# Kernel tuning notes

Measured on AMD Instinct MI355X. Metric: run time of the kernel, lower is better.

## Reference

```python
import jax, jax.numpy as jnp
import numpy as np

N = 50000
E = 800000
G = 256          # number of graphs in the batch
F_IN = 128
H1, D1 = 12, 32  # conv1: heads, out-per-head (concat -> 384)
H2, D2 = 1, 64   # conv2: single head
NEG_SLOPE = 0.2


def setup_inputs() -> dict:
    key = jax.random.key(0)
    ks = jax.random.split(key, 12)
    x = jax.random.normal(ks[0], (N, F_IN), dtype=jnp.float32)
    edge_index = jax.random.randint(ks[1], (2, E), 0, N, dtype=jnp.int64)
    batch = jnp.sort(jax.random.randint(ks[2], (N,), 0, G, dtype=jnp.int64))
    # conv1 params (Glorot-ish scaling)
    W1 = jax.random.normal(ks[3], (F_IN, H1 * D1), dtype=jnp.float32) * (1.0 / np.sqrt(F_IN))
    att_src1 = jax.random.normal(ks[4], (H1, D1), dtype=jnp.float32) * (1.0 / np.sqrt(D1))
    att_dst1 = jax.random.normal(ks[5], (H1, D1), dtype=jnp.float32) * (1.0 / np.sqrt(D1))
    bias1 = jnp.zeros((H1 * D1,), dtype=jnp.float32)
    # conv2 params
    W2 = jax.random.normal(ks[6], (H1 * D1, H2 * D2), dtype=jnp.float32) * (1.0 / np.sqrt(H1 * D1))
    att_src2 = jax.random.normal(ks[7], (H2, D2), dtype=jnp.float32) * (1.0 / np.sqrt(D2))
    att_dst2 = jax.random.normal(ks[8], (H2, D2), dtype=jnp.float32) * (1.0 / np.sqrt(D2))
    bias2 = jnp.zeros((H2 * D2,), dtype=jnp.float32)
    return {"x": x, "edge_index": edge_index, "batch": batch,
            "W1": W1, "att_src1": att_src1, "att_dst1": att_dst1, "bias1": bias1,
            "W2": W2, "att_src2": att_src2, "att_dst2": att_dst2, "bias2": bias2}


def gat_conv(x, src, dst, W, att_src, att_dst, bias, heads, d_out):
    # x: [N, F] -> h: [N, heads, d_out]
    h = (x @ W).reshape(N, heads, d_out)
    # per-node attention halves: [N, heads]
    a_src = jnp.einsum('nhd,hd->nh', h, att_src)
    a_dst = jnp.einsum('nhd,hd->nh', h, att_dst)
    # per-edge logits (edges include self-loops): [Etot, heads]
    e = jax.nn.leaky_relu(a_src[src] + a_dst[dst], NEG_SLOPE)
    # segment softmax over incoming edges of each destination node
    m = jax.ops.segment_max(e, dst, num_segments=N)          # [N, heads]
    e = jnp.exp(e - m[dst])
    s = jax.ops.segment_sum(e, dst, num_segments=N)          # [N, heads]
    alpha = e / s[dst]
    # weighted aggregation: [N, heads, d_out]
    out = jax.ops.segment_sum(alpha[:, :, None] * h[src], dst, num_segments=N)
    return out.reshape(N, heads * d_out) + bias


def reference(x, edge_index, batch, W1, att_src1, att_dst1, bias1,
              W2, att_src2, att_dst2, bias2):
    # add self-loops (PyG GATConv default add_self_loops=True)
    loops = jnp.arange(N, dtype=edge_index.dtype)
    src = jnp.concatenate([edge_index[0], loops])
    dst = jnp.concatenate([edge_index[1], loops])

    h = jax.nn.relu(gat_conv(x, src, dst, W1, att_src1, att_dst1, bias1, H1, D1))
    h = gat_conv(h, src, dst, W2, att_src2, att_dst2, bias2, H2, D2)

    # global mean pool over graphs
    sums = jax.ops.segment_sum(h, batch, num_segments=G)                 # [G, 64]
    cnts = jax.ops.segment_sum(jnp.ones((N,), h.dtype), batch, num_segments=G)
    return sums / jnp.maximum(cnts, 1.0)[:, None]
```

## Files before the change

kernel.cpp:

```cpp
#include <hip/hip_runtime.h>

#define N_NODES 50000
#define N_EDGES 800000
#define ETOT (N_EDGES + N_NODES)
#define G_GRAPHS 256
#define F_IN 128
#define H1 12
#define D1 32
#define C1 (H1*D1)
#define C2 64
#define NEG 0.2f
#define SCAN_B 1024
#define NBLK_SCAN ((N_NODES + SCAN_B - 1)/SCAN_B)

using bf16x8  = __attribute__((ext_vector_type(8))) short;
using ushort8 = __attribute__((ext_vector_type(8))) unsigned short;
using f32x4   = __attribute__((ext_vector_type(4))) float;

__device__ __forceinline__ float lrelu(float x){ return x > 0.f ? x : NEG*x; }
__device__ __forceinline__ unsigned short f2bf(float f){
  unsigned u = __float_as_uint(f);
  u += 0x7fffu + ((u >> 16) & 1u);
  return (unsigned short)(u >> 16);
}
__device__ __forceinline__ float bf2f(unsigned short h){
  return __uint_as_float(((unsigned)h) << 16);
}
__device__ __forceinline__ float wexp(float l){ return __expf(fminf(l, 30.f)); }

#define B_CAST ((N_NODES*F_IN/4 + 255)/256)
#define B_W1   ((F_IN*C1 + 255)/256)
#define B_W2   ((C1*C2 + 255)/256)
#define B_WAB  ((32*F_IN + 255)/256)
__global__ void prep_kernel(const float* __restrict__ x, const float* __restrict__ W1,
    const float* __restrict__ W2, const float* __restrict__ att_src,
    const float* __restrict__ att_dst, unsigned short* __restrict__ xb,
    unsigned short* __restrict__ w1t, unsigned short* __restrict__ w2t,
    unsigned short* __restrict__ wAb){
  int b = blockIdx.x, tid = threadIdx.x;
  if (b < B_CAST){
    int base = (b*256 + tid)*4;
    if (base >= N_NODES*F_IN) return;
    float4 v = *(const float4*)(x + base);
    ushort4 o; o.x=f2bf(v.x); o.y=f2bf(v.y); o.z=f2bf(v.z); o.w=f2bf(v.w);
    *(ushort4*)(xb + base) = o;
  } else if (b < B_CAST + B_W1){
    int i = (b - B_CAST)*256 + tid;
    if (i >= F_IN*C1) return;
    int n = i / F_IN, k = i % F_IN;
    w1t[i] = f2bf(W1[(size_t)k*C1 + n]);
  } else if (b < B_CAST + B_W1 + B_W2){
    int i = (b - B_CAST - B_W1)*256 + tid;
    if (i >= C1*C2) return;
    int n = i / C1, k = i % C1;
    w2t[i] = f2bf(W2[(size_t)k*C2 + n]);
  } else {
    int i = (b - B_CAST - B_W1 - B_W2)*256 + tid;
    if (i >= 32*F_IN) return;
    int c = i >> 7, k = i & 127;
    float v = 0.f;
    if (c < 12){
      #pragma unroll
      for (int dd=0; dd<D1; ++dd) v += W1[(size_t)k*C1 + c*D1 + dd] * att_src[c*D1 + dd];
    } else if (c < 24){
      int h = c - 12;
      #pragma unroll
      for (int dd=0; dd<D1; ++dd) v += W1[(size_t)k*C1 + h*D1 + dd] * att_dst[h*D1 + dd];
    }
    wAb[i] = f2bf(v);
  }
}

template<int BM,int BN,int WM,int WN,bool F32OUT>
__global__ __launch_bounds__(256) void gemm_mfma(const unsigned short* __restrict__ A,
    const unsigned short* __restrict__ Bt, void* __restrict__ Cv,
    int M, int N, int K){
  constexpr int BK = 32;
  __shared__ unsigned short As2[4][BM][8];
  __shared__ unsigned short Bs2[4][BN][8];
  const int tid  = threadIdx.x;
  const int wid  = tid >> 6, lane = tid & 63;
  constexpr int NWX = BN / WN;
  const int wrow = (wid / NWX) * WM, wcol = (wid % NWX) * WN;
  constexpr int MR = WM/16, NR = WN/16;
  const int row0 = blockIdx.x * BM, col0 = blockIdx.y * BN;
  const int r = lane & 15, koct = lane >> 4;
  f32x4 acc[MR][NR];
  #pragma unroll
  for (int m=0;m<MR;m++)
    #pragma unroll
    for (int n=0;n<NR;n++) acc[m][n] = f32x4{0.f,0.f,0.f,0.f};

  for (int k0 = 0; k0 < K; k0 += BK){
    for (int s = tid; s < BM*8; s += 256){
      int rr = s >> 3, cc = (s & 7) * 4;
      int gr = row0 + rr;
      ushort4 v = (gr < M) ? *(const ushort4*)(A + (size_t)gr*K + k0 + cc)
                           : ushort4{0,0,0,0};
      *(ushort4*)(&As2[cc>>3][rr][cc&7]) = v;
    }
    for (int s = tid; s < BN*8; s += 256){
      int rr = s >> 3, cc = (s & 7) * 4;
      ushort4 v = *(const ushort4*)(Bt + (size_t)(col0+rr)*K + k0 + cc);
      *(ushort4*)(&Bs2[cc>>3][rr][cc&7]) = v;
    }
    __syncthreads();
    bf16x8 af[MR], bq[NR];
    #pragma unroll
    for (int m=0;m<MR;m++) af[m] = *(const bf16x8*)(&As2[koct][wrow + m*16 + r][0]);
    #pragma unroll
    for (int n=0;n<NR;n++) bq[n] = *(const bf16x8*)(&Bs2[koct][wcol + n*16 + r][0]);
    #pragma unroll
    for (int m=0;m<MR;m++)
      #pragma unroll
      for (int n=0;n<NR;n++)
        acc[m][n] = __builtin_amdgcn_mfma_f32_16x16x32_bf16(af[m], bq[n], acc[m][n], 0,0,0);
    __syncthreads();
  }
  #pragma unroll
  for (int m=0;m<MR;m++){
    #pragma unroll
    for (int rr=0; rr<4; rr++){
      int grow = row0 + wrow + m*16 + koct*4 + rr;
      if (grow < M){
        #pragma unroll
        for (int n=0;n<NR;n++){
          if constexpr (F32OUT)
            ((float*)Cv)[(size_t)grow*N + col0 + wcol + n*16 + r] = acc[m][n][rr];
          else
            ((unsigned short*)Cv)[(size_t)grow*N + col0 + wcol + n*16 + r] = f2bf(acc[m][n][rr]);
        }
      }
    }
  }
}

#define EGRID ((ETOT + 255)/256)
#define NGRID ((N_NODES + 255)/256)
__global__ void count_cnt_kernel(const int* __restrict__ ei, const int* __restrict__ batch,
                                 int* __restrict__ counts, int* __restrict__ cnt){
  if ((int)blockIdx.x < EGRID){
    int e = blockIdx.x*256 + threadIdx.x;
    if (e >= ETOT) return;
    int d = (e < N_EDGES) ? ei[N_EDGES + e] : (e - N_EDGES);
    atomicAdd(&counts[d], 1);
  } else {
    int n = (blockIdx.x - EGRID)*256 + threadIdx.x;
    if (n < N_NODES) atomicAdd(&cnt[batch[n]], 1);
  }
}
__global__ __launch_bounds__(SCAN_B) void scan_pass1(const int* __restrict__ counts,
    int* __restrict__ excl, int* __restrict__ bsum){
  __shared__ int sdata[SCAN_B];
  int i = blockIdx.x*SCAN_B + threadIdx.x;
  int v = (i < N_NODES) ? counts[i] : 0;
  sdata[threadIdx.x] = v;
  __syncthreads();
  for (int off=1; off<SCAN_B; off<<=1){
    int t = (threadIdx.x >= off) ? sdata[threadIdx.x-off] : 0;
    __syncthreads();
    sdata[threadIdx.x] += t;
    __syncthreads();
  }
  if (i < N_NODES) excl[i] = sdata[threadIdx.x] - v;
  if (threadIdx.x == SCAN_B-1) bsum[blockIdx.x] = sdata[SCAN_B-1];
}
__global__ void scan_pass3(int* __restrict__ rowptr, const int* __restrict__ bsum,
                           int* __restrict__ cursor){
  __shared__ int carry_s;
  int sblk = blockIdx.x >> 2;
  if (threadIdx.x == 0){
    int c = 0;
    for (int b=0; b<sblk; ++b) c += bsum[b];
    carry_s = c;
  }
  __syncthreads();
  int i = blockIdx.x*256 + (int)threadIdx.x;
  if (i < N_NODES){
    int r = rowptr[i] + carry_s;
    rowptr[i] = r; cursor[i] = r;
  }
  if (i == N_NODES) rowptr[N_NODES] = ETOT;
}
__global__ void scatter_kernel(const int* __restrict__ ei, int* __restrict__ cursor,
                               int* __restrict__ csr_src){
  int e = blockIdx.x*blockDim.x + threadIdx.x;
  if (e >= ETOT) return;
  int s, d;
  if (e < N_EDGES){ s = ei[e]; d = ei[N_EDGES + e]; } else { s = d = e - N_EDGES; }
  int slot = atomicAdd(&cursor[d], 1);
  csr_src[slot] = s;
}

__global__ __launch_bounds__(256) void agg1g_kernel(const int* __restrict__ rowptr,
    const int* __restrict__ csr, const unsigned short* __restrict__ xb,
    const float* __restrict__ asd, const unsigned short* __restrict__ w1t,
    const unsigned short* __restrict__ w2t, const float* __restrict__ bias1,
    const float* __restrict__ att_src2, const float* __restrict__ att_dst2,
    unsigned short* __restrict__ h2, float* __restrict__ asrc2, float* __restrict__ adst2){
  constexpr int ROWE = 6*F_IN + 8;
  constexpr int WROW = 16*12 + 4;
  constexpr int ROWR = 192 + 8;
  __shared__ unsigned short agg[16*ROWE];
  __shared__ float wlds[16][WROW];

  unsigned short* reluLDS = (unsigned short*)&wlds[0][0];
  float* red = (float*)&agg[0];

  const int tid  = threadIdx.x;
  const int slot = tid >> 4;
  const int t16  = tid & 15;
  const int base = ((tid & 63) >> 4) * 16;
  const int d    = blockIdx.x*16 + slot;
  const int r0 = rowptr[d], r1 = rowptr[d+1];

  float4 ad0 = *(const float4*)(asd + (size_t)d*32 + 12);
  float4 ad1 = *(const float4*)(asd + (size_t)d*32 + 16);
  float4 ad2 = *(const float4*)(asd + (size_t)d*32 + 20);
  float ad[12] = {ad0.x,ad0.y,ad0.z,ad0.w, ad1.x,ad1.y,ad1.z,ad1.w, ad2.x,ad2.y,ad2.z,ad2.w};

  float acc[12][8];
  #pragma unroll
  for (int h=0;h<12;h++)
    #pragma unroll
    for (int i=0;i<8;i++) acc[h][i] = 0.f;
  float ss[12];
  #pragma unroll
  for (int h=0;h<12;h++) ss[h] = 0.f;

  for (int c0 = r0; c0 < r1; c0 += 16){
    int nc = min(16, r1 - c0);
    int s_st = 0;
    if (t16 < nc){
      int j = c0 + t16;
      s_st = csr[j];
      float4 s0 = *(const float4*)(asd + (size_t)s_st*32);
      float4 s1 = *(const float4*)(asd + (size_t)s_st*32 + 4);
      float4 s2 = *(const float4*)(asd + (size_t)s_st*32 + 8);
      float as[12] = {s0.x,s0.y,s0.z,s0.w, s1.x,s1.y,s1.z,s1.w, s2.x,s2.y,s2.z,s2.w};
      float w[12];
      #pragma unroll
      for (int h=0;h<12;h++){ w[h] = wexp(lrelu(as[h] + ad[h])); ss[h] += w[h]; }
      *(float4*)(&wlds[slot][t16*12 + 0]) = float4{w[0],w[1],w[2],w[3]};
      *(float4*)(&wlds[slot][t16*12 + 4]) = float4{w[4],w[5],w[6],w[7]};
      *(float4*)(&wlds[slot][t16*12 + 8]) = float4{w[8],w[9],w[10],w[11]};
    }
    __builtin_amdgcn_wave_barrier();
    int sA = __shfl(s_st, base + 0);
    ushort8 xA = *(const ushort8*)(xb + (size_t)sA*F_IN + t16*8);
    ushort8 xB = {0,0,0,0,0,0,0,0};
    if (nc > 1){
      int sB = __shfl(s_st, base + 1);
      xB = *(const ushort8*)(xb + (size_t)sB*F_IN + t16*8);
    }
    for (int e = 0; e < nc; ++e){
      ushort8 cx = xA;
      xA = xB;
      if (e + 2 < nc){
        int sN = __shfl(s_st, base + e + 2);
        xB = *(const ushort8*)(xb + (size_t)sN*F_IN + t16*8);
      }
      float4 w0 = *(const float4*)(&wlds[slot][e*12 + 0]);
      float4 w1 = *(const float4*)(&wlds[slot][e*12 + 4]);
      float4 w2 = *(const float4*)(&wlds[slot][e*12 + 8]);
      float xf[8];
      #pragma unroll
      for (int i=0;i<8;i++) xf[i] = bf2f((unsigned short)cx[i]);
      float w[12] = {w0.x,w0.y,w0.z,w0.w, w1.x,w1.y,w1.z,w1.w, w2.x,w2.y,w2.z,w2.w};
      #pragma unroll
      for (int h=0;h<12;h++)
        #pragma unroll
        for (int i=0;i<8;i++) acc[h][i] += w[h]*xf[i];
    }
    __builtin_amdgcn_wave_barrier();
  }

  #pragma unroll
  for (int h=0;h<12;h++){
    #pragma unroll
    for (int off=8; off; off>>=1) ss[h] += __shfl_xor(ss[h], off);
  }
  float inv[12];
  #pragma unroll
  for (int h=0;h<12;h++) inv[h] = 1.f / ss[h];

  const int wv = tid >> 6, wl = tid & 63;
  const int er = wl & 15, eq = wl >> 4;
  f32x4 h2acc = {0.f,0.f,0.f,0.f};
  #pragma unroll
  for (int hf = 0; hf < 2; ++hf){
    __syncthreads();
    #pragma unroll
    for (int h = 0; h < 6; ++h){
      int hh = hf*6 + h;
      ushort8 v;
      #pragma unroll
      for (int i=0;i<8;i++) v[i] = f2bf(acc[hh][i]*inv[hh]);
      *(ushort8*)(&agg[slot*ROWE + h*F_IN + t16*8]) = v;
    }
    __syncthreads();
    for (int tt = wv; tt < 12; tt += 4){
      int h = tt >> 1, nb = tt & 1;
      int hh = hf*6 + h;
      f32x4 c = {0.f,0.f,0.f,0.f};
      #pragma unroll
      for (int kk=0; kk<4; ++kk){
        bf16x8 af = *(const bf16x8*)(&agg[er*ROWE + h*F_IN + kk*32 + eq*8]);
        bf16x8 bq = *(const bf16x8*)(w1t + (size_t)(hh*32 + nb*16 + er)*F_IN + kk*32 + eq*8);
        c = __builtin_amdgcn_mfma_f32_16x16x32_bf16(af, bq, c, 0,0,0);
      }
      int lcol = tt*16 + er;
      float bv = bias1[hf*192 + lcol];
      #pragma unroll
      for (int rr=0; rr<4; ++rr){
        int row = eq*4 + rr;
        reluLDS[row*ROWR + lcol] = f2bf(fmaxf(c[rr] + bv, 0.f));
      }
    }
    __syncthreads();
    #pragma unroll
    for (int kk=0; kk<6; ++kk){
      bf16x8 af = *(const bf16x8*)(&reluLDS[er*ROWR + kk*32 + eq*8]);
      bf16x8 bq = *(const bf16x8*)(w2t + (size_t)(wv*16 + er)*C1 + hf*192 + kk*32 + eq*8);
      h2acc = __builtin_amdgcn_mfma_f32_16x16x32_bf16(af, bq, h2acc, 0,0,0);
    }
  }
  __syncthreads();

  float attS = att_src2[wv*16 + er];
  float attD = att_dst2[wv*16 + er];
  float psum[4], pdum[4];
  #pragma unroll
  for (int rr=0; rr<4; ++rr){
    int row = eq*4 + rr;
    int gn = blockIdx.x*16 + row;
    h2[(size_t)gn*C2 + wv*16 + er] = f2bf(h2acc[rr]);
    psum[rr] = h2acc[rr]*attS;
    pdum[rr] = h2acc[rr]*attD;
  }
  #pragma unroll
  for (int rr=0; rr<4; ++rr){
    #pragma unroll
    for (int off=8; off; off>>=1){
      psum[rr] += __shfl_xor(psum[rr], off);
      pdum[rr] += __shfl_xor(pdum[rr], off);
    }
  }
  if (er == 0){
    #pragma unroll
    for (int rr=0; rr<4; ++rr){
      int row = eq*4 + rr;
      red[(wv*16 + row)*2 + 0] = psum[rr];
      red[(wv*16 + row)*2 + 1] = pdum[rr];
    }
  }
  __syncthreads();
  if (tid < 32){
    int row = tid >> 1, which = tid & 1;
    float v = red[row*2+which] + red[(16+row)*2+which] + red[(32+row)*2+which] + red[(48+row)*2+which];
    int gn = blockIdx.x*16 + row;
    if (which == 0) asrc2[gn] = v; else adst2[gn] = v;
  }
}

__global__ __launch_bounds__(256) void agg2s_kernel(const int* __restrict__ rowptr,
    const int* __restrict__ csr, const unsigned short* __restrict__ h2,
    const float* __restrict__ asrc, const float* __restrict__ adst,
    const float* __restrict__ bias, const int* __restrict__ batch,
    float* __restrict__ pool){
  const int tid  = threadIdx.x;
  const int slot = tid >> 4;
  const int t16  = tid & 15;
  const int base = ((tid & 63) >> 4) * 16;
  const int d    = blockIdx.x*16 + slot;
  const int r0 = rowptr[d], r1 = rowptr[d+1];
  const float ad = adst[d];

  float ssp = 0.f;
  float a0=0.f, a1=0.f, a2=0.f, a3=0.f;

  for (int c0 = r0; c0 < r1; c0 += 16){
    int nc = min(16, r1 - c0);
    int s_st = 0; float w_st = 0.f;
    if (t16 < nc){
      s_st = csr[c0 + t16];
      w_st = wexp(lrelu(asrc[s_st] + ad));
      ssp += w_st;
    }
    int sA = __shfl(s_st, base + 0);
    ushort4 xA = *(const ushort4*)(h2 + (size_t)sA*C2 + t16*4);
    ushort4 xB = {0,0,0,0};
    if (nc > 1){
      int sB = __shfl(s_st, base + 1);
      xB = *(const ushort4*)(h2 + (size_t)sB*C2 + t16*4);
    }
    for (int e = 0; e < nc; ++e){
      ushort4 cx = xA;
      xA = xB;
      if (e + 2 < nc){
        int sN = __shfl(s_st, base + e + 2);
        xB = *(const ushort4*)(h2 + (size_t)sN*C2 + t16*4);
      }
      float w = __shfl(w_st, base + e);
      a0 += w*bf2f(cx.x);
      a1 += w*bf2f(cx.y);
      a2 += w*bf2f(cx.z);
      a3 += w*bf2f(cx.w);
    }
  }
  #pragma unroll
  for (int off=8; off; off>>=1) ssp += __shfl_xor(ssp, off);
  float inv = 1.f / ssp;
  int g = batch[d];
  int fb = t16*4;
  atomicAdd(&pool[g*C2 + fb+0], a0*inv + bias[fb+0]);
  atomicAdd(&pool[g*C2 + fb+1], a1*inv + bias[fb+1]);
  atomicAdd(&pool[g*C2 + fb+2], a2*inv + bias[fb+2]);
  atomicAdd(&pool[g*C2 + fb+3], a3*inv + bias[fb+3]);
}

__global__ void finalize_kernel(const float* __restrict__ sums, const int* __restrict__ cnt,
                                float* __restrict__ out){
  int i = blockIdx.x*blockDim.x + threadIdx.x;
  if (i >= G_GRAPHS*C2) return;
  int g = i >> 6;
  out[i] = sums[i] / fmaxf((float)cnt[g], 1.f);
}

extern "C" void kernel_launch(void* const* d_in, const int* in_sizes, int n_in,
                              void* d_out, int out_size, void* d_ws, size_t ws_size,
                              hipStream_t stream) {
  const float* x        = (const float*)d_in[0];
  const int*   ei       = (const int*)  d_in[1];
  const int*   batch    = (const int*)  d_in[2];
  const float* W1       = (const float*)d_in[3];
  const float* att_src1 = (const float*)d_in[4];
  const float* att_dst1 = (const float*)d_in[5];
  const float* bias1    = (const float*)d_in[6];
  const float* W2       = (const float*)d_in[7];
  const float* att_src2 = (const float*)d_in[8];
  const float* att_dst2 = (const float*)d_in[9];
  const float* bias2    = (const float*)d_in[10];
  float* out = (float*)d_out;

  char* ws = (char*)d_ws;
  size_t o = 0;
  auto alloc = [&](size_t bytes)->size_t{ size_t r=o; o=(o+bytes+255)&~(size_t)255; return r; };

  size_t xb_o     = alloc((size_t)N_NODES*F_IN*2);
  size_t w1t_o    = alloc((size_t)C1*F_IN*2);
  size_t w2t_o    = alloc((size_t)C2*C1*2);
  size_t wab_o    = alloc((size_t)32*F_IN*2);
  size_t asd_o    = alloc((size_t)N_NODES*32*4);
  size_t h2_o     = alloc((size_t)N_NODES*C2*2);
  size_t asrc2_o  = alloc((size_t)N_NODES*4);
  size_t adst2_o  = alloc((size_t)N_NODES*4);
  size_t zero_beg = o;
  size_t counts_o = alloc((size_t)N_NODES*4);
  size_t pool_o   = alloc((size_t)G_GRAPHS*C2*4);
  size_t cnt_o    = alloc((size_t)G_GRAPHS*4);
  size_t zero_end = o;
  size_t rowptr_o = alloc((size_t)(N_NODES+1)*4);
  size_t bsum_o   = alloc((size_t)NBLK_SCAN*4);
  size_t cursor_o = alloc((size_t)N_NODES*4);
  size_t csr_o    = alloc((size_t)ETOT*4);

  unsigned short* xb    = (unsigned short*)(ws + xb_o);
  unsigned short* w1t   = (unsigned short*)(ws + w1t_o);
  unsigned short* w2t   = (unsigned short*)(ws + w2t_o);
  unsigned short* wab   = (unsigned short*)(ws + wab_o);
  float* asd    = (float*)(ws + asd_o);
  unsigned short* h2b   = (unsigned short*)(ws + h2_o);
  float* asrc2  = (float*)(ws + asrc2_o);
  float* adst2  = (float*)(ws + adst2_o);
  int*   counts = (int*)  (ws + counts_o);
  float* poolf  = (float*)(ws + pool_o);
  int*   cnt    = (int*)  (ws + cnt_o);
  int*   rowptr = (int*)  (ws + rowptr_o);
  int*   bsum   = (int*)  (ws + bsum_o);
  int*   cursor = (int*)  (ws + cursor_o);
  int*   csrsrc = (int*)  (ws + csr_o);

  hipMemsetAsync(ws + zero_beg, 0, zero_end - zero_beg, stream);

  const int TPB = 256;

  prep_kernel<<<B_CAST + B_W1 + B_W2 + B_WAB, TPB, 0, stream>>>(
      x, W1, W2, att_src1, att_dst1, xb, w1t, w2t, wab);

  count_cnt_kernel<<<EGRID + NGRID, TPB, 0, stream>>>(ei, batch, counts, cnt);
  scan_pass1<<<NBLK_SCAN, SCAN_B, 0, stream>>>(counts, rowptr, bsum);
  scan_pass3<<<(N_NODES + 1 + 255)/256, TPB, 0, stream>>>(rowptr, bsum, cursor);
  scatter_kernel<<<EGRID, TPB, 0, stream>>>(ei, cursor, csrsrc);

  gemm_mfma<64,32,32,16,true><<<dim3((N_NODES+63)/64, 1), 256, 0, stream>>>(xb, wab, asd, N_NODES, 32, F_IN);
  agg1g_kernel<<<N_NODES/16, 256, 0, stream>>>(rowptr, csrsrc, xb, asd, w1t, w2t,
                                               bias1, att_src2, att_dst2, h2b, asrc2, adst2);
  agg2s_kernel<<<(N_NODES+15)/16, TPB, 0, stream>>>(rowptr, csrsrc, h2b, asrc2, adst2, bias2, batch, poolf);

  finalize_kernel<<<(G_GRAPHS*C2 + TPB-1)/TPB, TPB, 0, stream>>>(poolf, cnt, out);
}
```

Baseline: 424.4 us.

## Use MFMA for conv1 edge aggregation with one wave per destination node

The layer-1 aggregation kernel now assigns one 64-lane wave per destination node (1024-thread blocks, 16 nodes each) instead of 16 lanes per node. Each wave processes 32 edges per chunk. Gathered source features are transposed into swizzled LDS and reduced against bf16 attention weights with 16x16x32 bf16 MFMAs, replacing the scalar FMA accumulation over 12 heads by 8 features. The goal is to move the dominant per-edge weighted-sum work onto matrix cores. In exchange, attention weights are rounded to bf16, LDS use per block grows a lot, and zero-padding waste appears for low-degree nodes.

```diff
diff --git a/kernel.cpp b/kernel.cpp
--- a/kernel.cpp
+++ b/kernel.cpp
@@ -192,172 +192,188 @@
   csr_src[slot] = s;
 }
 
-__global__ __launch_bounds__(256) void agg1g_kernel(const int* __restrict__ rowptr,
+__global__ __launch_bounds__(1024) void agg1m_kernel(const int* __restrict__ rowptr,
     const int* __restrict__ csr, const unsigned short* __restrict__ xb,
     const float* __restrict__ asd, const unsigned short* __restrict__ w1t,
     const unsigned short* __restrict__ w2t, const float* __restrict__ bias1,
     const float* __restrict__ att_src2, const float* __restrict__ att_dst2,
     unsigned short* __restrict__ h2, float* __restrict__ asrc2, float* __restrict__ adst2){
-  constexpr int ROWE = 6*F_IN + 8;
-  constexpr int WROW = 16*12 + 4;
-  constexpr int ROWR = 192 + 8;
-  __shared__ unsigned short agg[16*ROWE];
-  __shared__ float wlds[16][WROW];
-
-  unsigned short* reluLDS = (unsigned short*)&wlds[0][0];
-  float* red = (float*)&agg[0];
+  __shared__ unsigned short XtU[16*128*32];
+  __shared__ unsigned short wldsU[16*16*32];
+  unsigned short* aggU  = XtU;
+  unsigned short* reluU = wldsU;
+  float* redF = (float*)&wldsU[7168];
 
   const int tid  = threadIdx.x;
-  const int slot = tid >> 4;
-  const int t16  = tid & 15;
-  const int base = ((tid & 63) >> 4) * 16;
-  const int d    = blockIdx.x*16 + slot;
+  const int wv   = tid >> 6;
+  const int lane = tid & 63;
+  const int e32  = lane & 31, half = lane >> 5;
+  const int r    = lane & 15, koct = lane >> 4;
+  const int d    = blockIdx.x*16 + wv;
   const int r0 = rowptr[d], r1 = rowptr[d+1];
+  const int wvX = wv * (128*32);
+  const int wvW = wv * (16*32);
+
+  if (lane < 32){
+    #pragma unroll
+    for (int h=12; h<16; ++h) wldsU[wvW + h*32 + lane] = 0;
+  }
 
   float4 ad0 = *(const float4*)(asd + (size_t)d*32 + 12);
   float4 ad1 = *(const float4*)(asd + (size_t)d*32 + 16);
   float4 ad2 = *(const float4*)(asd + (size_t)d*32 + 20);
   float ad[12] = {ad0.x,ad0.y,ad0.z,ad0.w, ad1.x,ad1.y,ad1.z,ad1.w, ad2.x,ad2.y,ad2.z,ad2.w};
 
-  float acc[12][8];
-  #pragma unroll
-  for (int h=0;h<12;h++)
-    #pragma unroll
-    for (int i=0;i<8;i++) acc[h][i] = 0.f;
+  f32x4 c[8];
+  #pragma unroll
+  for (int t=0;t<8;t++) c[t] = f32x4{0.f,0.f,0.f,0.f};
   float ss[12];
   #pragma unroll
   for (int h=0;h<12;h++) ss[h] = 0.f;
 
-  for (int c0 = r0; c0 < r1; c0 += 16){
-    int nc = min(16, r1 - c0);
+  for (int c0 = r0; c0 < r1; c0 += 32){
+    int nc = min(32, r1 - c0);
     int s_st = 0;
-    if (t16 < nc){
-      int j = c0 + t16;
-      s_st = csr[j];
-      float4 s0 = *(const float4*)(asd + (size_t)s_st*32);
-      float4 s1 = *(const float4*)(asd + (size_t)s_st*32 + 4);
-      float4 s2 = *(const float4*)(asd + (size_t)s_st*32 + 8);
-      float as[12] = {s0.x,s0.y,s0.z,s0.w, s1.x,s1.y,s1.z,s1.w, s2.x,s2.y,s2.z,s2.w};
-      float w[12];
-      #pragma unroll
-      for (int h=0;h<12;h++){ w[h] = wexp(lrelu(as[h] + ad[h])); ss[h] += w[h]; }
-      *(float4*)(&wlds[slot][t16*12 + 0]) = float4{w[0],w[1],w[2],w[3]};
-      *(float4*)(&wlds[slot][t16*12 + 4]) = float4{w[4],w[5],w[6],w[7]};
-      *(float4*)(&wlds[slot][t16*12 + 8]) = float4{w[8],w[9],w[10],w[11]};
+    if (lane < 32){
+      if (lane < nc){
+        s_st = csr[c0 + lane];
+        float4 s0 = *(const float4*)(asd + (size_t)s_st*32);
+        float4 s1 = *(const float4*)(asd + (size_t)s_st*32 + 4);
+        float4 s2 = *(const float4*)(asd + (size_t)s_st*32 + 8);
+        float as[12] = {s0.x,s0.y,s0.z,s0.w, s1.x,s1.y,s1.z,s1.w, s2.x,s2.y,s2.z,s2.w};
+        #pragma unroll
+        for (int h=0;h<12;h++){
+          unsigned short wb = f2bf(wexp(lrelu(as[h] + ad[h])));
+          wldsU[wvW + h*32 + lane] = wb;
+          ss[h] += bf2f(wb);
+        }
+      } else {
+        #pragma unroll
+        for (int h=0;h<12;h++) wldsU[wvW + h*32 + lane] = 0;
+      }
     }
     __builtin_amdgcn_wave_barrier();
-    int sA = __shfl(s_st, base + 0);
-    ushort8 xA = *(const ushort8*)(xb + (size_t)sA*F_IN + t16*8);
-    ushort8 xB = {0,0,0,0,0,0,0,0};
-    if (nc > 1){
-      int sB = __shfl(s_st, base + 1);
-      xB = *(const ushort8*)(xb + (size_t)sB*F_IN + t16*8);
-    }
-    for (int e = 0; e < nc; ++e){
-      ushort8 cx = xA;
-      xA = xB;
-      if (e + 2 < nc){
-        int sN = __shfl(s_st, base + e + 2);
-        xB = *(const ushort8*)(xb + (size_t)sN*F_IN + t16*8);
-      }
-      float4 w0 = *(const float4*)(&wlds[slot][e*12 + 0]);
-      float4 w1 = *(const float4*)(&wlds[slot][e*12 + 4]);
-      float4 w2 = *(const float4*)(&wlds[slot][e*12 + 8]);
-      float xf[8];
-      #pragma unroll
-      for (int i=0;i<8;i++) xf[i] = bf2f((unsigned short)cx[i]);
-      float w[12] = {w0.x,w0.y,w0.z,w0.w, w1.x,w1.y,w1.z,w1.w, w2.x,w2.y,w2.z,w2.w};
-      #pragma unroll
-      for (int h=0;h<12;h++)
+    asm volatile("" ::: "memory");
+    int s = __shfl(s_st, e32);
+    ushort8 xv0,xv1,xv2,xv3,xv4,xv5,xv6,xv7;
+    if (e32 < nc){
+      const unsigned short* xp = xb + (size_t)s*F_IN + half*64;
+      xv0 = *(const ushort8*)(xp);      xv1 = *(const ushort8*)(xp+8);
+      xv2 = *(const ushort8*)(xp+16);   xv3 = *(const ushort8*)(xp+24);
+      xv4 = *(const ushort8*)(xp+32);   xv5 = *(const ushort8*)(xp+40);
+      xv6 = *(const ushort8*)(xp+48);   xv7 = *(const ushort8*)(xp+56);
+    } else {
+      xv0=xv1=xv2=xv3=xv4=xv5=xv6=xv7 = ushort8{0,0,0,0,0,0,0,0};
+    }
+    {
+      int ebase = wvX + (e32 & 7);
+      int echunk = e32 >> 3;
+      #pragma unroll
+      for (int i=0;i<8;i++){
+        ushort8 xv = (i==0)?xv0:(i==1)?xv1:(i==2)?xv2:(i==3)?xv3:(i==4)?xv4:(i==5)?xv5:(i==6)?xv6:xv7;
         #pragma unroll
-        for (int i=0;i<8;i++) acc[h][i] += w[h]*xf[i];
-    }
+        for (int j=0;j<8;j++){
+          int f = half*64 + i*8 + j;
+          XtU[ebase + f*32 + (((echunk + f)&3)<<3)] = (unsigned short)xv[j];
+        }
+      }
+    }
+    asm volatile("" ::: "memory");
     __builtin_amdgcn_wave_barrier();
+    bf16x8 bq = *(const bf16x8*)&wldsU[wvW + r*32 + koct*8];
+    #pragma unroll
+    for (int t=0;t<8;t++){
+      int feat = t*16 + r;
+      bf16x8 af = *(const bf16x8*)&XtU[wvX + feat*32 + (((koct + feat)&3)<<3)];
+      c[t] = __builtin_amdgcn_mfma_f32_16x16x32_bf16(af, bq, c[t], 0,0,0);
+    }
+    asm volatile("" ::: "memory");
+    __builtin_amdgcn_wave_barrier();
   }
 
   #pragma unroll
   for (int h=0;h<12;h++){
     #pragma unroll
-    for (int off=8; off; off>>=1) ss[h] += __shfl_xor(ss[h], off);
-  }
-  float inv[12];
-  #pragma unroll
-  for (int h=0;h<12;h++) inv[h] = 1.f / ss[h];
-
-  const int wv = tid >> 6, wl = tid & 63;
-  const int er = wl & 15, eq = wl >> 4;
-  f32x4 h2acc = {0.f,0.f,0.f,0.f};
-  #pragma unroll
-  for (int hf = 0; hf < 2; ++hf){
-    __syncthreads();
-    #pragma unroll
-    for (int h = 0; h < 6; ++h){
-      int hh = hf*6 + h;
-      ushort8 v;
-      #pragma unroll
-      for (int i=0;i<8;i++) v[i] = f2bf(acc[hh][i]*inv[hh]);
-      *(ushort8*)(&agg[slot*ROWE + h*F_IN + t16*8]) = v;
-    }
-    __syncthreads();
-    for (int tt = wv; tt < 12; tt += 4){
-      int h = tt >> 1, nb = tt & 1;
-      int hh = hf*6 + h;
-      f32x4 c = {0.f,0.f,0.f,0.f};
-      #pragma unroll
-      for (int kk=0; kk<4; ++kk){
-        bf16x8 af = *(const bf16x8*)(&agg[er*ROWE + h*F_IN + kk*32 + eq*8]);
-        bf16x8 bq = *(const bf16x8*)(w1t + (size_t)(hh*32 + nb*16 + er)*F_IN + kk*32 + eq*8);
-        c = __builtin_amdgcn_mfma_f32_16x16x32_bf16(af, bq, c, 0,0,0);
-      }
-      int lcol = tt*16 + er;
-      float bv = bias1[hf*192 + lcol];
+    for (int off=32; off; off>>=1) ss[h] += __shfl_xor(ss[h], off);
+  }
+  float invr = 0.f;
+  #pragma unroll
+  for (int h=0;h<12;h++){ float iv = 1.f/ss[h]; invr = (r==h) ? iv : invr; }
+
+  __syncthreads();
+
+  if (r < 12){
+    #pragma unroll
+    for (int t=0;t<8;t++){
+      #pragma unroll
+      for (int rr=0;rr<4;rr++){
+        int feat = t*16 + koct*4 + rr;
+        aggU[wv*1640 + r*136 + feat] = f2bf(c[t][rr] * invr);
+      }
+    }
+  }
+  __syncthreads();
+
+  for (int tt = wv; tt < 24; tt += 16){
+    int h = tt >> 1, nb = tt & 1;
+    f32x4 cw = {0.f,0.f,0.f,0.f};
+    #pragma unroll
+    for (int kk=0; kk<4; ++kk){
+      bf16x8 af = *(const bf16x8*)&aggU[r*1640 + h*136 + kk*32 + koct*8];
+      bf16x8 bq = *(const bf16x8*)(w1t + (size_t)(h*32 + nb*16 + r)*F_IN + kk*32 + koct*8);
+      cw = __builtin_amdgcn_mfma_f32_16x16x32_bf16(af, bq, cw, 0,0,0);
+    }
+    int col = h*32 + nb*16 + r;
+    float bv = bias1[col];
+    #pragma unroll
+    for (int rr=0; rr<4; ++rr){
+      int row = koct*4 + rr;
+      reluU[row*392 + col] = f2bf(fmaxf(cw[rr] + bv, 0.f));
+    }
+  }
+  __syncthreads();
+
+  if (wv < 4){
+    f32x4 h2acc = {0.f,0.f,0.f,0.f};
+    #pragma unroll
+    for (int kk=0; kk<12; ++kk){
+      bf16x8 af = *(const bf16x8*)&reluU[r*392 + kk*32 + koct*8];
+      bf16x8 bq = *(const bf16x8*)(w2t + (size_t)(wv*16 + r)*C1 + kk*32 + koct*8);
+      h2acc = __builtin_amdgcn_mfma_f32_16x16x32_bf16(af, bq, h2acc, 0,0,0);
+    }
+    float attS = att_src2[wv*16 + r];
+    float attD = att_dst2[wv*16 + r];
+    float psum[4], pdum[4];
+    #pragma unroll
+    for (int rr=0; rr<4; ++rr){
+      int row = koct*4 + rr;
+      int gn = blockIdx.x*16 + row;
+      h2[(size_t)gn*C2 + wv*16 + r] = f2bf(h2acc[rr]);
+      psum[rr] = h2acc[rr]*attS;
+      pdum[rr] = h2acc[rr]*attD;
+    }
+    #pragma unroll
+    for (int rr=0; rr<4; ++rr){
+      #pragma unroll
+      for (int off=8; off; off>>=1){
+        psum[rr] += __shfl_xor(psum[rr], off);
+        pdum[rr] += __shfl_xor(pdum[rr], off);
+      }
+    }
+    if (r == 0){
       #pragma unroll
       for (int rr=0; rr<4; ++rr){
-        int row = eq*4 + rr;
-        reluLDS[row*ROWR + lcol] = f2bf(fmaxf(c[rr] + bv, 0.f));
-      }
-    }
-    __syncthreads();
-    #pragma unroll
-    for (int kk=0; kk<6; ++kk){
-      bf16x8 af = *(const bf16x8*)(&reluLDS[er*ROWR + kk*32 + eq*8]);
-      bf16x8 bq = *(const bf16x8*)(w2t + (size_t)(wv*16 + er)*C1 + hf*192 + kk*32 + eq*8);
-      h2acc = __builtin_amdgcn_mfma_f32_16x16x32_bf16(af, bq, h2acc, 0,0,0);
-    }
-  }
-  __syncthreads();
-
-  float attS = att_src2[wv*16 + er];
-  float attD = att_dst2[wv*16 + er];
-  float psum[4], pdum[4];
-  #pragma unroll
-  for (int rr=0; rr<4; ++rr){
-    int row = eq*4 + rr;
-    int gn = blockIdx.x*16 + row;
-    h2[(size_t)gn*C2 + wv*16 + er] = f2bf(h2acc[rr]);
-    psum[rr] = h2acc[rr]*attS;
-    pdum[rr] = h2acc[rr]*attD;
-  }
-  #pragma unroll
-  for (int rr=0; rr<4; ++rr){
-    #pragma unroll
-    for (int off=8; off; off>>=1){
-      psum[rr] += __shfl_xor(psum[rr], off);
-      pdum[rr] += __shfl_xor(pdum[rr], off);
-    }
-  }
-  if (er == 0){
-    #pragma unroll
-    for (int rr=0; rr<4; ++rr){
-      int row = eq*4 + rr;
-      red[(wv*16 + row)*2 + 0] = psum[rr];
-      red[(wv*16 + row)*2 + 1] = pdum[rr];
+        int row = koct*4 + rr;
+        redF[(wv*16 + row)*2 + 0] = psum[rr];
+        redF[(wv*16 + row)*2 + 1] = pdum[rr];
+      }
     }
   }
   __syncthreads();
   if (tid < 32){
     int row = tid >> 1, which = tid & 1;
-    float v = red[row*2+which] + red[(16+row)*2+which] + red[(32+row)*2+which] + red[(48+row)*2+which];
+    float v = redF[row*2+which] + redF[(16+row)*2+which]
+            + redF[(32+row)*2+which] + redF[(48+row)*2+which];
     int gn = blockIdx.x*16 + row;
     if (which == 0) asrc2[gn] = v; else adst2[gn] = v;
   }
@@ -494,8 +510,8 @@
   scatter_kernel<<<EGRID, TPB, 0, stream>>>(ei, cursor, csrsrc);
 
   gemm_mfma<64,32,32,16,true><<<dim3((N_NODES+63)/64, 1), 256, 0, stream>>>(xb, wab, asd, N_NODES, 32, F_IN);
-  agg1g_kernel<<<N_NODES/16, 256, 0, stream>>>(rowptr, csrsrc, xb, asd, w1t, w2t,
-                                               bias1, att_src2, att_dst2, h2b, asrc2, adst2);
+  agg1m_kernel<<<N_NODES/16, 1024, 0, stream>>>(rowptr, csrsrc, xb, asd, w1t, w2t,
+                                                bias1, att_src2, att_dst2, h2b, asrc2, adst2);
   agg2s_kernel<<<(N_NODES+15)/16, TPB, 0, stream>>>(rowptr, csrsrc, h2b, asrc2, adst2, bias2, batch, poolf);
 
   finalize_kernel<<<(G_GRAPHS*C2 + TPB-1)/TPB, TPB, 0, stream>>>(poolf, cnt, out);
```

After: 453.0 us. 6.7% more time.

## Precompute per-edge attention weights in separate kernel and deepen gather prefetch

Applied to the files above, without the earlier changes.

Adds a wprep kernel that computes the 12 per-head exp(leakyrelu) edge weights once per CSR edge and stores them as bf16, using a new csr_dst array written by the scatter kernel. The conv1 aggregation kernel then loads these precomputed weights instead of gathering source and destination attention scores and computing exponentials inline. Both aggregation kernels also move from a 2-deep to a 3-deep register prefetch of gathered feature rows. The cost is an extra kernel launch, about 20 MB of extra weight traffic plus the csr_dst array, bf16 rounding of the softmax weights, and more register pressure.

```diff
diff --git a/kernel.cpp b/kernel.cpp
--- a/kernel.cpp
+++ b/kernel.cpp
@@ -183,18 +183,41 @@
   if (i == N_NODES) rowptr[N_NODES] = ETOT;
 }
 __global__ void scatter_kernel(const int* __restrict__ ei, int* __restrict__ cursor,
-                               int* __restrict__ csr_src){
+                               int* __restrict__ csr_src, int* __restrict__ csr_dst){
   int e = blockIdx.x*blockDim.x + threadIdx.x;
   if (e >= ETOT) return;
   int s, d;
   if (e < N_EDGES){ s = ei[e]; d = ei[N_EDGES + e]; } else { s = d = e - N_EDGES; }
   int slot = atomicAdd(&cursor[d], 1);
   csr_src[slot] = s;
+  csr_dst[slot] = d;
+}
+
+__global__ void wprep_kernel(const int* __restrict__ csr, const int* __restrict__ csrd,
+                             const float* __restrict__ asd, unsigned short* __restrict__ walpha){
+  int j = blockIdx.x*256 + threadIdx.x;
+  if (j >= ETOT) return;
+  int s = csr[j], d = csrd[j];
+  float4 s0 = *(const float4*)(asd + (size_t)s*32);
+  float4 s1 = *(const float4*)(asd + (size_t)s*32 + 4);
+  float4 s2 = *(const float4*)(asd + (size_t)s*32 + 8);
+  float4 d0 = *(const float4*)(asd + (size_t)d*32 + 12);
+  float4 d1 = *(const float4*)(asd + (size_t)d*32 + 16);
+  float4 d2 = *(const float4*)(asd + (size_t)d*32 + 20);
+  float as[12] = {s0.x,s0.y,s0.z,s0.w, s1.x,s1.y,s1.z,s1.w, s2.x,s2.y,s2.z,s2.w};
+  float ad[12] = {d0.x,d0.y,d0.z,d0.w, d1.x,d1.y,d1.z,d1.w, d2.x,d2.y,d2.z,d2.w};
+  unsigned short wb[12];
+  #pragma unroll
+  for (int h=0;h<12;h++) wb[h] = f2bf(wexp(lrelu(as[h] + ad[h])));
+  unsigned short* wp = walpha + (size_t)j*12;
+  *(ushort4*)(wp)   = ushort4{wb[0],wb[1],wb[2],wb[3]};
+  *(ushort4*)(wp+4) = ushort4{wb[4],wb[5],wb[6],wb[7]};
+  *(ushort4*)(wp+8) = ushort4{wb[8],wb[9],wb[10],wb[11]};
 }
 
 __global__ __launch_bounds__(256) void agg1g_kernel(const int* __restrict__ rowptr,
     const int* __restrict__ csr, const unsigned short* __restrict__ xb,
-    const float* __restrict__ asd, const unsigned short* __restrict__ w1t,
+    const unsigned short* __restrict__ walpha, const unsigned short* __restrict__ w1t,
     const unsigned short* __restrict__ w2t, const float* __restrict__ bias1,
     const float* __restrict__ att_src2, const float* __restrict__ att_dst2,
     unsigned short* __restrict__ h2, float* __restrict__ asrc2, float* __restrict__ adst2){
@@ -214,11 +237,6 @@
   const int d    = blockIdx.x*16 + slot;
   const int r0 = rowptr[d], r1 = rowptr[d+1];
 
-  float4 ad0 = *(const float4*)(asd + (size_t)d*32 + 12);
-  float4 ad1 = *(const float4*)(asd + (size_t)d*32 + 16);
-  float4 ad2 = *(const float4*)(asd + (size_t)d*32 + 20);
-  float ad[12] = {ad0.x,ad0.y,ad0.z,ad0.w, ad1.x,ad1.y,ad1.z,ad1.w, ad2.x,ad2.y,ad2.z,ad2.w};
-
   float acc[12][8];
   #pragma unroll
   for (int h=0;h<12;h++)
@@ -234,13 +252,15 @@
     if (t16 < nc){
       int j = c0 + t16;
       s_st = csr[j];
-      float4 s0 = *(const float4*)(asd + (size_t)s_st*32);
-      float4 s1 = *(const float4*)(asd + (size_t)s_st*32 + 4);
-      float4 s2 = *(const float4*)(asd + (size_t)s_st*32 + 8);
-      float as[12] = {s0.x,s0.y,s0.z,s0.w, s1.x,s1.y,s1.z,s1.w, s2.x,s2.y,s2.z,s2.w};
-      float w[12];
-      #pragma unroll
-      for (int h=0;h<12;h++){ w[h] = wexp(lrelu(as[h] + ad[h])); ss[h] += w[h]; }
+      const unsigned short* wp = walpha + (size_t)j*12;
+      ushort4 u0 = *(const ushort4*)(wp);
+      ushort4 u1 = *(const ushort4*)(wp+4);
+      ushort4 u2 = *(const ushort4*)(wp+8);
+      float w[12] = {bf2f(u0.x),bf2f(u0.y),bf2f(u0.z),bf2f(u0.w),
+                     bf2f(u1.x),bf2f(u1.y),bf2f(u1.z),bf2f(u1.w),
+                     bf2f(u2.x),bf2f(u2.y),bf2f(u2.z),bf2f(u2.w)};
+      #pragma unroll
+      for (int h=0;h<12;h++) ss[h] += w[h];
       *(float4*)(&wlds[slot][t16*12 + 0]) = float4{w[0],w[1],w[2],w[3]};
       *(float4*)(&wlds[slot][t16*12 + 4]) = float4{w[4],w[5],w[6],w[7]};
       *(float4*)(&wlds[slot][t16*12 + 8]) = float4{w[8],w[9],w[10],w[11]};
@@ -248,17 +268,21 @@
     __builtin_amdgcn_wave_barrier();
     int sA = __shfl(s_st, base + 0);
     ushort8 xA = *(const ushort8*)(xb + (size_t)sA*F_IN + t16*8);
-    ushort8 xB = {0,0,0,0,0,0,0,0};
+    ushort8 xB = {0,0,0,0,0,0,0,0}, xC = {0,0,0,0,0,0,0,0};
     if (nc > 1){
       int sB = __shfl(s_st, base + 1);
       xB = *(const ushort8*)(xb + (size_t)sB*F_IN + t16*8);
     }
+    if (nc > 2){
+      int sC = __shfl(s_st, base + 2);
+      xC = *(const ushort8*)(xb + (size_t)sC*F_IN + t16*8);
+    }
     for (int e = 0; e < nc; ++e){
       ushort8 cx = xA;
-      xA = xB;
-      if (e + 2 < nc){
-        int sN = __shfl(s_st, base + e + 2);
-        xB = *(const ushort8*)(xb + (size_t)sN*F_IN + t16*8);
+      xA = xB; xB = xC;
+      if (e + 3 < nc){
+        int sN = __shfl(s_st, base + e + 3);
+        xC = *(const ushort8*)(xb + (size_t)sN*F_IN + t16*8);
       }
       float4 w0 = *(const float4*)(&wlds[slot][e*12 + 0]);
       float4 w1 = *(const float4*)(&wlds[slot][e*12 + 4]);
@@ -389,17 +413,21 @@
     }
     int sA = __shfl(s_st, base + 0);
     ushort4 xA = *(const ushort4*)(h2 + (size_t)sA*C2 + t16*4);
-    ushort4 xB = {0,0,0,0};
+    ushort4 xB = {0,0,0,0}, xC = {0,0,0,0};
     if (nc > 1){
       int sB = __shfl(s_st, base + 1);
       xB = *(const ushort4*)(h2 + (size_t)sB*C2 + t16*4);
     }
+    if (nc > 2){
+      int sC = __shfl(s_st, base + 2);
+      xC = *(const ushort4*)(h2 + (size_t)sC*C2 + t16*4);
+    }
     for (int e = 0; e < nc; ++e){
       ushort4 cx = xA;
-      xA = xB;
-      if (e + 2 < nc){
-        int sN = __shfl(s_st, base + e + 2);
-        xB = *(const ushort4*)(h2 + (size_t)sN*C2 + t16*4);
+      xA = xB; xB = xC;
+      if (e + 3 < nc){
+        int sN = __shfl(s_st, base + e + 3);
+        xC = *(const ushort4*)(h2 + (size_t)sN*C2 + t16*4);
       }
       float w = __shfl(w_st, base + e);
       a0 += w*bf2f(cx.x);
@@ -455,6 +483,7 @@
   size_t h2_o     = alloc((size_t)N_NODES*C2*2);
   size_t asrc2_o  = alloc((size_t)N_NODES*4);
   size_t adst2_o  = alloc((size_t)N_NODES*4);
+  size_t walpha_o = alloc((size_t)ETOT*12*2);
   size_t zero_beg = o;
   size_t counts_o = alloc((size_t)N_NODES*4);
   size_t pool_o   = alloc((size_t)G_GRAPHS*C2*4);
@@ -464,6 +493,7 @@
   size_t bsum_o   = alloc((size_t)NBLK_SCAN*4);
   size_t cursor_o = alloc((size_t)N_NODES*4);
   size_t csr_o    = alloc((size_t)ETOT*4);
+  size_t csrd_o   = alloc((size_t)ETOT*4);
 
   unsigned short* xb    = (unsigned short*)(ws + xb_o);
   unsigned short* w1t   = (unsigned short*)(ws + w1t_o);
@@ -473,6 +503,7 @@
   unsigned short* h2b   = (unsigned short*)(ws + h2_o);
   float* asrc2  = (float*)(ws + asrc2_o);
   float* adst2  = (float*)(ws + adst2_o);
+  unsigned short* walpha = (unsigned short*)(ws + walpha_o);
   int*   counts = (int*)  (ws + counts_o);
   float* poolf  = (float*)(ws + pool_o);
   int*   cnt    = (int*)  (ws + cnt_o);
@@ -480,6 +511,7 @@
   int*   bsum   = (int*)  (ws + bsum_o);
   int*   cursor = (int*)  (ws + cursor_o);
   int*   csrsrc = (int*)  (ws + csr_o);
+  int*   csrdst = (int*)  (ws + csrd_o);
 
   hipMemsetAsync(ws + zero_beg, 0, zero_end - zero_beg, stream);
 
@@ -491,10 +523,11 @@
   count_cnt_kernel<<<EGRID + NGRID, TPB, 0, stream>>>(ei, batch, counts, cnt);
   scan_pass1<<<NBLK_SCAN, SCAN_B, 0, stream>>>(counts, rowptr, bsum);
   scan_pass3<<<(N_NODES + 1 + 255)/256, TPB, 0, stream>>>(rowptr, bsum, cursor);
-  scatter_kernel<<<EGRID, TPB, 0, stream>>>(ei, cursor, csrsrc);
+  scatter_kernel<<<EGRID, TPB, 0, stream>>>(ei, cursor, csrsrc, csrdst);
 
   gemm_mfma<64,32,32,16,true><<<dim3((N_NODES+63)/64, 1), 256, 0, stream>>>(xb, wab, asd, N_NODES, 32, F_IN);
-  agg1g_kernel<<<N_NODES/16, 256, 0, stream>>>(rowptr, csrsrc, xb, asd, w1t, w2t,
+  wprep_kernel<<<EGRID, TPB, 0, stream>>>(csrsrc, csrdst, asd, walpha);
+  agg1g_kernel<<<N_NODES/16, TPB, 0, stream>>>(rowptr, csrsrc, xb, walpha, w1t, w2t,
                                                bias1, att_src2, att_dst2, h2b, asrc2, adst2);
   agg2s_kernel<<<(N_NODES+15)/16, TPB, 0, stream>>>(rowptr, csrsrc, h2b, asrc2, adst2, bias2, batch, poolf);
 
```

Measured after the change: 418.7 us. No clear change (-1.3%).
